# Kernel tuning notes

Hardware: AMD Instinct MI355X
Metric: run time of the kernel (lower is better)

The kernel has to match this reference:

```python
import jax, jax.numpy as jnp
import numpy as np

B, L, D, K, V = 256, 50, 128, 4, 50000
LENGTH = 5      # opt.length
BETA = 0.01     # opt.beta scaling on loss1
EPS = 1e-12     # F.normalize eps


def _l2norm(x, axis):
    n = jnp.sqrt(jnp.sum(x * x, axis=axis, keepdims=True))
    return x / jnp.maximum(n, EPS)


def setup_inputs() -> dict:
    key = jax.random.key(0)
    ks = jax.random.split(key, 11)
    s = 1.0 / np.sqrt(D)  # reset_parameters: uniform(-stdv, stdv)
    u = lambda k, shape: jax.random.uniform(k, shape, jnp.float32, -s, s)
    return {
        "hidden": jax.random.normal(ks[0], (B, L, D), jnp.float32),
        "mask": jnp.ones((B, L), jnp.int32),
        "pos_emb": u(ks[1], (L, D)),
        "w1": u(ks[2], (2 * D, D)),
        "w2": u(ks[3], (D, K)),
        "glu1_w": u(ks[4], (D, K * D)),
        "glu1_b": u(ks[5], (K * D,)),
        "att_w1": u(ks[6], (D, D)),
        "att_w2": u(ks[7], (D, D)),
        "att_v": u(ks[8], (D, K)),
        "emb": u(ks[9], (V, D)),
    }


def reference(hidden, mask, pos_emb, w1, w2, glu1_w, glu1_b, att_w1, att_w2, att_v, emb):
    m = mask.astype(jnp.float32)[..., None]                       # [B,L,1]
    hs = jnp.sum(hidden * m, axis=1) / jnp.sum(m, axis=1)         # [B,D] masked mean
    # nh = tanh(cat(pos, hidden) @ w1); then sigmoid(glu1)
    cat = jnp.concatenate([jnp.broadcast_to(pos_emb[None], hidden.shape), hidden], axis=-1)
    nh = jnp.tanh(cat @ w1)                                       # [B,L,D]
    nh = jax.nn.sigmoid(nh @ glu1_w + glu1_b)                     # [B,L,K*D]
    # torch.split(dim=2) + stack(dim=3) -> [B,L,D,K]
    nh = nh.reshape(B, L, K, D).transpose(0, 1, 3, 2)             # [B,L,D,K]
    beta = jnp.einsum('bldk,dk->blk', nh, w2)                     # [B,L,K]
    # attention gate alpha = sigmoid(att_v(tanh(W1 hs + W2 hidden)))
    att = jnp.tanh(hs[:, None, :] @ att_w1 + hidden @ att_w2)     # [B,L,D]
    alpha = jax.nn.sigmoid(att @ att_v)                           # [B,L,K]
    beta = beta * (0.5 + alpha) * m                               # mask over interests
    # per-interest L2 normalize along sequence (fused over K)
    nb = _l2norm(beta, axis=1)                                    # [B,L,K]
    # pairwise |cos| between interests: vectorized Gram instead of python loops
    G = jnp.einsum('bli,blj->bij', nb, nb)                        # [B,K,K]
    triu = jnp.triu(jnp.ones((K, K), jnp.float32), 1)
    sim = jnp.sum(jnp.abs(G) * triu, axis=(1, 2)) * (2.0 / (K * (K - 1)))  # [B]
    lens = jnp.sum(mask, axis=1).astype(jnp.float32) - LENGTH     # sumask[:,0] - length
    loss1 = jnp.sum(jax.nn.sigmoid(sim * lens))                   # scalar
    # per-interest pooled session reps, stacked on leading axis -> [K,B,D]
    select = jnp.einsum('blk,bld->kbd', beta, hidden)
    b_norm = _l2norm(emb[1:], axis=-1)                            # [V-1,D]
    scores = jnp.einsum('kbd,vd->kbv', select, b_norm)            # [K,B,V-1]
    max_scores = jnp.max(scores, axis=0)                          # [B,V-1]
    return (max_scores, loss1 * BETA, scores)
```

## Files before the change

### kernel.cpp

```cpp
#include <hip/hip_runtime.h>
#include <hip/hip_bf16.h>
#include <math.h>

constexpr int NB = 256;
constexpr int NL = 50;
constexpr int ND = 128;
constexpr int NK = 4;
constexpr int NVm1 = 49999;
constexpr int NPAD2 = 50176;
constexpr int ROWS = NB * NL;
constexpr int MROWS = NB * NK;
constexpr int GEMM_NSPAN = 512;
constexpr int MR = 64;

constexpr int G_BN  = NPAD2 / 8;
constexpr int G_HS  = NB / 2;
constexpr int G_PP  = NL / 2;
constexpr int G_XB  = ROWS * ND / 2048;
constexpr int G_W1T = ND * ND / 256;
constexpr int G_AWT = ND * ND / 256;
constexpr int G_GLT = ND * 512 / 256;
constexpr int G_TOT = G_BN + G_HS + G_PP + G_XB + G_W1T + G_AWT + G_GLT;

typedef __bf16 bf16x8 __attribute__((ext_vector_type(8)));
typedef float f32x4 __attribute__((ext_vector_type(4)));

__device__ __forceinline__ float sigm_fast(float x) { return 1.0f / (1.0f + __expf(-x)); }
__device__ __forceinline__ float sigm_prec(float x) { return 1.0f / (1.0f + expf(-x)); }
__device__ __forceinline__ float fast_tanh(float x) {
    float xc = fminf(fmaxf(x, -15.f), 15.f);
    float e = __expf(2.f * xc);
    return (e - 1.f) / (e + 1.f);
}

__device__ __forceinline__ void gld_lds16(const void* g, void* l) {
    __builtin_amdgcn_global_load_lds(
        (const __attribute__((address_space(1))) void*)g,
        (__attribute__((address_space(3))) void*)l, 16, 0, 0);
}

__global__ __launch_bounds__(256) void k_prep(
    const float* __restrict__ hidden, const int* __restrict__ mask,
    const float* __restrict__ pos_emb, const float* __restrict__ w1,
    const float* __restrict__ att_w2, const float* __restrict__ glu1_w,
    const float* __restrict__ emb,
    float* __restrict__ hs, float* __restrict__ posPart,
    __hip_bfloat16* __restrict__ XbG, __hip_bfloat16* __restrict__ w1h_t,
    __hip_bfloat16* __restrict__ attw2_t, __hip_bfloat16* __restrict__ glu_t,
    __hip_bfloat16* __restrict__ bnv, float* __restrict__ loss_out) {
    __shared__ float sPP[2 * ND];
    int blk = blockIdx.x, tid = threadIdx.x;
    if (blk < G_BN) {
        int v = blk * 8 + (tid >> 5);
        int j = (tid & 31) << 2;
        float4 x = make_float4(0.f, 0.f, 0.f, 0.f);
        if (v < NVm1) x = *(const float4*)&emb[((size_t)v + 1) * ND + j];
        float ss = x.x * x.x + x.y * x.y + x.z * x.z + x.w * x.w;
#pragma unroll
        for (int off = 16; off >= 1; off >>= 1) ss += __shfl_xor(ss, off);
        float rn = 1.f / fmaxf(sqrtf(ss), 1e-12f);
        union { ushort4 u4; __hip_bfloat16 h[4]; } o;
        o.h[0] = __float2bfloat16(x.x * rn);
        o.h[1] = __float2bfloat16(x.y * rn);
        o.h[2] = __float2bfloat16(x.z * rn);
        o.h[3] = __float2bfloat16(x.w * rn);
        *(ushort4*)&bnv[(size_t)v * ND + j] = o.u4;
    } else if (blk < G_BN + G_HS) {
        int b = (blk - G_BN) * 2 + (tid >> 7);
        int d = tid & 127;
        float acc = 0.f, msum = 0.f;
        for (int l = 0; l < NL; ++l) {
            float mv = (float)mask[b * NL + l];
            acc += hidden[((size_t)b * NL + l) * ND + d] * mv;
            msum += mv;
        }
        hs[b * ND + d] = acc / msum;
        if (blk == G_BN && tid == 0) loss_out[0] = 0.f;
    } else if (blk < G_BN + G_HS + G_PP) {
        int rel = blk - (G_BN + G_HS);
        int rl = tid >> 7, d = tid & 127;
        int r = rel * 2 + rl;
        sPP[rl * ND + d] = pos_emb[r * ND + d];
        __syncthreads();
        float acc = 0.f;
#pragma unroll 8
        for (int j = 0; j < ND; ++j) acc += sPP[rl * ND + j] * w1[j * ND + d];
        posPart[r * ND + d] = acc;
    } else if (blk < G_BN + G_HS + G_PP + G_XB) {
        int rel = blk - (G_BN + G_HS + G_PP);
        size_t base = (size_t)rel * 2048 + (size_t)tid * 8;
        float4 f0 = *(const float4*)&hidden[base];
        float4 f1 = *(const float4*)&hidden[base + 4];
        union { bf16x8 v; __hip_bfloat16 h[8]; } u;
        u.h[0] = __float2bfloat16(f0.x); u.h[1] = __float2bfloat16(f0.y);
        u.h[2] = __float2bfloat16(f0.z); u.h[3] = __float2bfloat16(f0.w);
        u.h[4] = __float2bfloat16(f1.x); u.h[5] = __float2bfloat16(f1.y);
        u.h[6] = __float2bfloat16(f1.z); u.h[7] = __float2bfloat16(f1.w);
        *(bf16x8*)&XbG[base] = u.v;
    } else if (blk < G_BN + G_HS + G_PP + G_XB + G_W1T) {
        int i = (blk - (G_BN + G_HS + G_PP + G_XB)) * 256 + tid;
        int d = i >> 7, j = i & 127;
        w1h_t[d * ND + j] = __float2bfloat16(w1[(ND + j) * ND + d]);
    } else if (blk < G_BN + G_HS + G_PP + G_XB + G_W1T + G_AWT) {
        int i = (blk - (G_BN + G_HS + G_PP + G_XB + G_W1T)) * 256 + tid;
        int d = i >> 7, j = i & 127;
        attw2_t[d * ND + j] = __float2bfloat16(att_w2[j * ND + d]);
    } else {
        int i = (blk - (G_BN + G_HS + G_PP + G_XB + G_W1T + G_AWT)) * 256 + tid;
        int c = i >> 7, j = i & 127;
        glu_t[c * ND + j] = __float2bfloat16(glu1_w[j * 512 + c]);
    }
}

__global__ __launch_bounds__(256) void k_mega(
    const __hip_bfloat16* __restrict__ XbG, const __hip_bfloat16* __restrict__ w1h_t,
    const __hip_bfloat16* __restrict__ attw2_t, const __hip_bfloat16* __restrict__ glu_t,
    const float* __restrict__ hs, const float* __restrict__ att_w1,
    const float* __restrict__ att_v, const float* __restrict__ posPart,
    const float* __restrict__ glu1_b, const float* __restrict__ w2,
    const int* __restrict__ mask, float* __restrict__ beta_out) {
    __shared__ __hip_bfloat16 XbS[MR * ND];
    __shared__ __hip_bfloat16 WS[ND * ND];
    __shared__ __attribute__((aligned(16))) __hip_bfloat16 NHS[MR * 136];
    __shared__ float alphaS[MR * NK];
    __shared__ float hsW1S[3 * ND];
    int row0 = blockIdx.x * MR;
    int tid = threadIdx.x;
    int wave = tid >> 6, lane = tid & 63, l16 = lane & 15, quad = lane >> 4;
    int b0 = row0 / NL;

#pragma unroll
    for (int it = 0; it < 4; ++it) {
        int id = it * 256 + tid;
        int row = id >> 4, c = id & 15, gc = c ^ (row & 7);
        gld_lds16((const char*)XbG + ((size_t)(row0 + row) * 16 + gc) * 16,
                  (char*)XbS + (size_t)(it * 256 + wave * 64) * 16);
    }
#pragma unroll
    for (int it = 0; it < 8; ++it) {
        int id = it * 256 + tid;
        int row = id >> 4, c = id & 15, gc = c ^ (row & 7);
        gld_lds16((const char*)attw2_t + ((size_t)row * 16 + gc) * 16,
                  (char*)WS + (size_t)(it * 256 + wave * 64) * 16);
    }
    for (int i = tid; i < 3 * ND; i += 256) {
        int bb = i >> 7, d = i & 127, b = b0 + bb;
        float acc = 0.f;
        if (b < NB) {
            for (int j = 0; j < ND; ++j) acc += hs[b * ND + j] * att_w1[j * ND + d];
        }
        hsW1S[i] = acc;
    }
    __syncthreads();

    const bf16x8* Xv = (const bf16x8*)XbS;
    const bf16x8* Wv = (const bf16x8*)WS;
    const bf16x8* Nv = (const bf16x8*)NHS;
    int arow = wave * 16 + l16;

    f32x4 acc8[8];
#pragma unroll
    for (int ni = 0; ni < 8; ++ni) acc8[ni] = (f32x4){0.f, 0.f, 0.f, 0.f};
#pragma unroll
    for (int kk = 0; kk < 4; ++kk) {
        int ko = kk * 4 + quad;
        bf16x8 af = Xv[arow * 16 + (ko ^ (arow & 7))];
#pragma unroll
        for (int ni = 0; ni < 8; ++ni) {
            int n = ni * 16 + l16;
            bf16x8 bf = Wv[n * 16 + (ko ^ (n & 7))];
            acc8[ni] = __builtin_amdgcn_mfma_f32_16x16x32_bf16(af, bf, acc8[ni], 0, 0, 0);
        }
    }
#pragma unroll
    for (int r = 0; r < 4; ++r) {
        int lrow = wave * 16 + quad * 4 + r;
        int grow = row0 + lrow;
        int bb = grow / NL - b0;
        float a0 = 0.f, a1 = 0.f, a2 = 0.f, a3 = 0.f;
#pragma unroll
        for (int ni = 0; ni < 8; ++ni) {
            int col = ni * 16 + l16;
            float atv = fast_tanh(hsW1S[bb * ND + col] + acc8[ni][r]);
            float4 av = *(const float4*)&att_v[col * 4];
            a0 += atv * av.x; a1 += atv * av.y; a2 += atv * av.z; a3 += atv * av.w;
        }
#pragma unroll
        for (int off = 1; off < 16; off <<= 1) {
            a0 += __shfl_xor(a0, off); a1 += __shfl_xor(a1, off);
            a2 += __shfl_xor(a2, off); a3 += __shfl_xor(a3, off);
        }
        if (l16 == 0) {
            alphaS[lrow * 4 + 0] = sigm_fast(a0);
            alphaS[lrow * 4 + 1] = sigm_fast(a1);
            alphaS[lrow * 4 + 2] = sigm_fast(a2);
            alphaS[lrow * 4 + 3] = sigm_fast(a3);
        }
    }
    __syncthreads();
#pragma unroll
    for (int it = 0; it < 8; ++it) {
        int id = it * 256 + tid;
        int row = id >> 4, c = id & 15, gc = c ^ (row & 7);
        gld_lds16((const char*)w1h_t + ((size_t)row * 16 + gc) * 16,
                  (char*)WS + (size_t)(it * 256 + wave * 64) * 16);
    }
    __syncthreads();
#pragma unroll
    for (int ni = 0; ni < 8; ++ni) acc8[ni] = (f32x4){0.f, 0.f, 0.f, 0.f};
#pragma unroll
    for (int kk = 0; kk < 4; ++kk) {
        int ko = kk * 4 + quad;
        bf16x8 af = Xv[arow * 16 + (ko ^ (arow & 7))];
#pragma unroll
        for (int ni = 0; ni < 8; ++ni) {
            int n = ni * 16 + l16;
            bf16x8 bf = Wv[n * 16 + (ko ^ (n & 7))];
            acc8[ni] = __builtin_amdgcn_mfma_f32_16x16x32_bf16(af, bf, acc8[ni], 0, 0, 0);
        }
    }
#pragma unroll
    for (int r = 0; r < 4; ++r) {
        int lrow = wave * 16 + quad * 4 + r;
        int grow = row0 + lrow;
        int l = grow % NL;
#pragma unroll
        for (int ni = 0; ni < 8; ++ni) {
            int col = ni * 16 + l16;
            float nhv = fast_tanh(posPart[l * ND + col] + acc8[ni][r]);
            NHS[lrow * 136 + col] = __float2bfloat16(nhv);
        }
    }
    __syncthreads();
    for (int ch = 0; ch < 4; ++ch) {
#pragma unroll
        for (int it = 0; it < 8; ++it) {
            int id = it * 256 + tid;
            int row = id >> 4, c = id & 15, gc = c ^ (row & 7);
            gld_lds16((const char*)glu_t + ((size_t)(ch * ND + row) * 16 + gc) * 16,
                      (char*)WS + (size_t)(it * 256 + wave * 64) * 16);
        }
        __syncthreads();
#pragma unroll
        for (int ni = 0; ni < 8; ++ni) acc8[ni] = (f32x4){0.f, 0.f, 0.f, 0.f};
#pragma unroll
        for (int kk = 0; kk < 4; ++kk) {
            int ko = kk * 4 + quad;
            bf16x8 af = Nv[arow * 17 + ko];
#pragma unroll
            for (int ni = 0; ni < 8; ++ni) {
                int n = ni * 16 + l16;
                bf16x8 bf = Wv[n * 16 + (ko ^ (n & 7))];
                acc8[ni] = __builtin_amdgcn_mfma_f32_16x16x32_bf16(af, bf, acc8[ni], 0, 0, 0);
            }
        }
#pragma unroll
        for (int r = 0; r < 4; ++r) {
            float s = 0.f;
#pragma unroll
            for (int ni = 0; ni < 8; ++ni) {
                int col = ni * 16 + l16;
                s += sigm_fast(acc8[ni][r] + glu1_b[ch * ND + col]) * w2[col * 4 + ch];
            }
#pragma unroll
            for (int off = 1; off < 16; off <<= 1) s += __shfl_xor(s, off);
            if (l16 == 0) {
                int lrow = wave * 16 + quad * 4 + r;
                int grow = row0 + lrow;
                float a = alphaS[lrow * 4 + ch];
                beta_out[(size_t)grow * 4 + ch] = s * (0.5f + a) * (float)mask[grow];
            }
        }
        __syncthreads();
    }
}

__global__ void k_loss(const float* __restrict__ beta, const int* __restrict__ mask,
                       float* __restrict__ loss_out) {
    int b = blockIdx.x;
    int t = threadIdx.x;
    float mv = (t < NL) ? (float)mask[b * NL + t] : 0.f;
    float msum = mv;
    for (int off = 32; off >= 1; off >>= 1) msum += __shfl_xor(msum, off);
    float lens = msum - 5.0f;
    float bk[NK] = {0.f, 0.f, 0.f, 0.f};
    if (t < NL) {
#pragma unroll
        for (int k = 0; k < NK; ++k) bk[k] = beta[((size_t)b * NL + t) * NK + k];
    }
    float nb[NK];
#pragma unroll
    for (int k = 0; k < NK; ++k) {
        float v = bk[k] * bk[k];
        for (int off = 32; off >= 1; off >>= 1) v += __shfl_xor(v, off);
        nb[k] = bk[k] / fmaxf(sqrtf(v), 1e-12f);
    }
    float sim = 0.f;
#pragma unroll
    for (int i = 0; i < NK; ++i) {
#pragma unroll
        for (int j = 0; j < NK; ++j) {
            if (j > i) {
                float p = nb[i] * nb[j];
                for (int off = 32; off >= 1; off >>= 1) p += __shfl_xor(p, off);
                sim += fabsf(p);
            }
        }
    }
    sim *= (2.0f / (NK * (NK - 1)));
    if (t == 0) atomicAdd(loss_out, sigm_prec(sim * lens) * 0.01f);
}

__global__ __launch_bounds__(256) void k_select(
    const float* __restrict__ beta, const float* __restrict__ hidden,
    __hip_bfloat16* __restrict__ selb) {
    int b = blockIdx.x * 2 + (threadIdx.x >> 7);
    int d = threadIdx.x & 127;
    float a0 = 0.f, a1 = 0.f, a2 = 0.f, a3 = 0.f;
    for (int l = 0; l < NL; ++l) {
        float h = hidden[((size_t)b * NL + l) * ND + d];
        float4 bv = *(const float4*)&beta[((size_t)b * NL + l) * NK];
        a0 = fmaf(bv.x, h, a0);
        a1 = fmaf(bv.y, h, a1);
        a2 = fmaf(bv.z, h, a2);
        a3 = fmaf(bv.w, h, a3);
    }
    selb[((size_t)b * NK + 0) * ND + d] = __float2bfloat16(a0);
    selb[((size_t)b * NK + 1) * ND + d] = __float2bfloat16(a1);
    selb[((size_t)b * NK + 2) * ND + d] = __float2bfloat16(a2);
    selb[((size_t)b * NK + 3) * ND + d] = __float2bfloat16(a3);
}

__global__ __launch_bounds__(256) void k_gemm(
    const __hip_bfloat16* __restrict__ selb, const __hip_bfloat16* __restrict__ bn,
    float* __restrict__ scores, float* __restrict__ maxs) {
    __shared__ __attribute__((aligned(16))) __hip_bfloat16 As[128 * 128];
    __shared__ __attribute__((aligned(16))) __hip_bfloat16 Bs[2][64 * 128];
    int bm0 = blockIdx.y * 128;
    int nbase = blockIdx.x * GEMM_NSPAN;
    int tid = threadIdx.x;
    int wave = tid >> 6, lane = tid & 63;
    int l16 = lane & 15, quad = lane >> 4;
    int m_loc = wave * 32;
    bool full = (nbase + GEMM_NSPAN) <= NVm1;
    const size_t SC_K = (size_t)NB * NVm1;

#pragma unroll
    for (int it = 0; it < 8; ++it) {
        int id = it * 256 + tid;
        int row = id >> 4, c = id & 15, gc = c ^ (row & 7);
        gld_lds16((const char*)selb + ((size_t)(bm0 + row) * 16 + gc) * 16,
                  (char*)As + (size_t)(it * 256 + wave * 64) * 16);
    }
#pragma unroll
    for (int it = 0; it < 4; ++it) {
        int id = it * 256 + tid;
        int row = id >> 4, c = id & 15, gc = c ^ (row & 7);
        gld_lds16((const char*)bn + ((size_t)(nbase + row) * 16 + gc) * 16,
                  (char*)Bs[0] + (size_t)(it * 256 + wave * 64) * 16);
    }
    __syncthreads();

    const bf16x8* Av = (const bf16x8*)As;

#pragma unroll
    for (int ch = 0; ch < 8; ++ch) {
        if (ch < 7) {
            int bn0 = nbase + (ch + 1) * 64;
#pragma unroll
            for (int it = 0; it < 4; ++it) {
                int id = it * 256 + tid;
                int row = id >> 4, c = id & 15, gc = c ^ (row & 7);
                gld_lds16((const char*)bn + ((size_t)(bn0 + row) * 16 + gc) * 16,
                          (char*)Bs[(ch + 1) & 1] + (size_t)(it * 256 + wave * 64) * 16);
            }
            __builtin_amdgcn_sched_barrier(0);
        }
        const bf16x8* Bv = (const bf16x8*)Bs[ch & 1];
        f32x4 acc[2][4];
#pragma unroll
        for (int mi = 0; mi < 2; ++mi)
#pragma unroll
            for (int ni = 0; ni < 4; ++ni) acc[mi][ni] = (f32x4){0.f, 0.f, 0.f, 0.f};

#pragma unroll
        for (int kk = 0; kk < 4; ++kk) {
            int ko = kk * 4 + quad;
            bf16x8 afr[2], bfr[4];
#pragma unroll
            for (int mi = 0; mi < 2; ++mi) {
                int row = m_loc + mi * 16 + l16;
                afr[mi] = Av[row * 16 + (ko ^ (row & 7))];
            }
#pragma unroll
            for (int ni = 0; ni < 4; ++ni) {
                int row = ni * 16 + l16;
                bfr[ni] = Bv[row * 16 + (ko ^ (row & 7))];
            }
#pragma unroll
            for (int mi = 0; mi < 2; ++mi)
#pragma unroll
                for (int ni = 0; ni < 4; ++ni)
                    acc[mi][ni] = __builtin_amdgcn_mfma_f32_16x16x32_bf16(
                        afr[mi], bfr[ni], acc[mi][ni], 0, 0, 0);
        }

        int ncol0 = nbase + ch * 64;
#pragma unroll
        for (int mi = 0; mi < 2; ++mi) {
            int m_base = bm0 + m_loc + mi * 16;
            int bidx = (m_base >> 2) + quad;
#pragma unroll
            for (int ni = 0; ni < 4; ++ni) {
                int n = ncol0 + ni * 16 + l16;
                if (full || n < NVm1) {
                    float mx = acc[mi][ni][0];
#pragma unroll
                    for (int r = 0; r < 4; ++r) {
                        float val = acc[mi][ni][r];
                        scores[(size_t)r * SC_K + (size_t)bidx * NVm1 + n] = val;
                        mx = fmaxf(mx, val);
                    }
                    maxs[(size_t)bidx * NVm1 + n] = mx;
                }
            }
        }

        if (ch < 7) {
            if (full) {
                asm volatile("s_waitcnt vmcnt(40) lgkmcnt(0)" ::: "memory");
                __builtin_amdgcn_s_barrier();
            } else {
                __syncthreads();
            }
        }
    }
}

extern "C" void kernel_launch(void* const* d_in, const int* in_sizes, int n_in,
                              void* d_out, int out_size, void* d_ws, size_t ws_size,
                              hipStream_t stream) {
    const float* hidden  = (const float*)d_in[0];
    const int*   mask    = (const int*)d_in[1];
    const float* pos_emb = (const float*)d_in[2];
    const float* w1      = (const float*)d_in[3];
    const float* w2      = (const float*)d_in[4];
    const float* glu1_w  = (const float*)d_in[5];
    const float* glu1_b  = (const float*)d_in[6];
    const float* att_w1  = (const float*)d_in[7];
    const float* att_w2  = (const float*)d_in[8];
    const float* att_v   = (const float*)d_in[9];
    const float* emb     = (const float*)d_in[10];

    float* out      = (float*)d_out;
    float* max_out  = out;
    float* loss_out = out + (size_t)NB * NVm1;
    float* scores   = out + (size_t)NB * NVm1 + 1;

    char* w = (char*)d_ws;
    auto alloc = [&](size_t bytes) {
        char* p = w;
        w += (bytes + 255) & ~(size_t)255;
        return p;
    };
    float* posPart = (float*)alloc((size_t)NL * ND * 4);
    float* hs      = (float*)alloc((size_t)NB * ND * 4);
    float* betav   = (float*)alloc((size_t)ROWS * NK * 4);
    __hip_bfloat16* XbG     = (__hip_bfloat16*)alloc((size_t)ROWS * ND * 2);
    __hip_bfloat16* w1h_t   = (__hip_bfloat16*)alloc((size_t)ND * ND * 2);
    __hip_bfloat16* attw2_t = (__hip_bfloat16*)alloc((size_t)ND * ND * 2);
    __hip_bfloat16* glu_t   = (__hip_bfloat16*)alloc((size_t)512 * ND * 2);
    __hip_bfloat16* selb    = (__hip_bfloat16*)alloc((size_t)MROWS * ND * 2);
    __hip_bfloat16* bnv     = (__hip_bfloat16*)alloc((size_t)NPAD2 * ND * 2);

    k_prep<<<G_TOT, 256, 0, stream>>>(hidden, mask, pos_emb, w1, att_w2, glu1_w, emb,
                                      hs, posPart, XbG, w1h_t, attw2_t, glu_t, bnv, loss_out);
    k_mega<<<ROWS / MR, 256, 0, stream>>>(XbG, w1h_t, attw2_t, glu_t, hs, att_w1,
                                          att_v, posPart, glu1_b, w2, mask, betav);
    k_loss<<<NB, 64, 0, stream>>>(betav, mask, loss_out);
    k_select<<<NB / 2, 256, 0, stream>>>(betav, hidden, selb);
    k_gemm<<<dim3(NPAD2 / GEMM_NSPAN, MROWS / 128), 256, 0, stream>>>(selb, bnv, scores, max_out);
}
```

Baseline: 432.4 us.

## Precompute hs@att_w1 in prep; restructure score GEMM with swapped operands and vector stores

```diff
diff --git a/kernel.cpp b/kernel.cpp
--- a/kernel.cpp
+++ b/kernel.cpp
@@ -14,16 +14,17 @@
 constexpr int MR = 64;
 
 constexpr int G_BN  = NPAD2 / 8;
-constexpr int G_HS  = NB / 2;
+constexpr int G_HW  = NB / 2;
 constexpr int G_PP  = NL / 2;
 constexpr int G_XB  = ROWS * ND / 2048;
 constexpr int G_W1T = ND * ND / 256;
 constexpr int G_AWT = ND * ND / 256;
 constexpr int G_GLT = ND * 512 / 256;
-constexpr int G_TOT = G_BN + G_HS + G_PP + G_XB + G_W1T + G_AWT + G_GLT;
+constexpr int G_TOT = G_BN + G_HW + G_PP + G_XB + G_W1T + G_AWT + G_GLT;
 
 typedef __bf16 bf16x8 __attribute__((ext_vector_type(8)));
 typedef float f32x4 __attribute__((ext_vector_type(4)));
+typedef f32x4 f32x4u __attribute__((aligned(4)));
 
 __device__ __forceinline__ float sigm_fast(float x) { return 1.0f / (1.0f + __expf(-x)); }
 __device__ __forceinline__ float sigm_prec(float x) { return 1.0f / (1.0f + expf(-x)); }
@@ -42,9 +43,9 @@
 __global__ __launch_bounds__(256) void k_prep(
     const float* __restrict__ hidden, const int* __restrict__ mask,
     const float* __restrict__ pos_emb, const float* __restrict__ w1,
-    const float* __restrict__ att_w2, const float* __restrict__ glu1_w,
-    const float* __restrict__ emb,
-    float* __restrict__ hs, float* __restrict__ posPart,
+    const float* __restrict__ att_w1, const float* __restrict__ att_w2,
+    const float* __restrict__ glu1_w, const float* __restrict__ emb,
+    float* __restrict__ hsW1, float* __restrict__ posPart,
     __hip_bfloat16* __restrict__ XbG, __hip_bfloat16* __restrict__ w1h_t,
     __hip_bfloat16* __restrict__ attw2_t, __hip_bfloat16* __restrict__ glu_t,
     __hip_bfloat16* __restrict__ bnv, float* __restrict__ loss_out) {
@@ -65,19 +66,24 @@
         o.h[2] = __float2bfloat16(x.z * rn);
         o.h[3] = __float2bfloat16(x.w * rn);
         *(ushort4*)&bnv[(size_t)v * ND + j] = o.u4;
-    } else if (blk < G_BN + G_HS) {
-        int b = (blk - G_BN) * 2 + (tid >> 7);
-        int d = tid & 127;
+    } else if (blk < G_BN + G_HW) {
+        int half = tid >> 7, d = tid & 127;
+        int b = (blk - G_BN) * 2 + half;
         float acc = 0.f, msum = 0.f;
         for (int l = 0; l < NL; ++l) {
             float mv = (float)mask[b * NL + l];
             acc += hidden[((size_t)b * NL + l) * ND + d] * mv;
             msum += mv;
         }
-        hs[b * ND + d] = acc / msum;
+        sPP[half * ND + d] = acc / msum;
+        __syncthreads();
+        float o = 0.f;
+#pragma unroll 8
+        for (int j = 0; j < ND; ++j) o += sPP[half * ND + j] * att_w1[j * ND + d];
+        hsW1[b * ND + d] = o;
         if (blk == G_BN && tid == 0) loss_out[0] = 0.f;
-    } else if (blk < G_BN + G_HS + G_PP) {
-        int rel = blk - (G_BN + G_HS);
+    } else if (blk < G_BN + G_HW + G_PP) {
+        int rel = blk - (G_BN + G_HW);
         int rl = tid >> 7, d = tid & 127;
         int r = rel * 2 + rl;
         sPP[rl * ND + d] = pos_emb[r * ND + d];
@@ -86,8 +92,8 @@
 #pragma unroll 8
         for (int j = 0; j < ND; ++j) acc += sPP[rl * ND + j] * w1[j * ND + d];
         posPart[r * ND + d] = acc;
-    } else if (blk < G_BN + G_HS + G_PP + G_XB) {
-        int rel = blk - (G_BN + G_HS + G_PP);
+    } else if (blk < G_BN + G_HW + G_PP + G_XB) {
+        int rel = blk - (G_BN + G_HW + G_PP);
         size_t base = (size_t)rel * 2048 + (size_t)tid * 8;
         float4 f0 = *(const float4*)&hidden[base];
         float4 f1 = *(const float4*)&hidden[base + 4];
@@ -97,16 +103,16 @@
         u.h[4] = __float2bfloat16(f1.x); u.h[5] = __float2bfloat16(f1.y);
         u.h[6] = __float2bfloat16(f1.z); u.h[7] = __float2bfloat16(f1.w);
         *(bf16x8*)&XbG[base] = u.v;
-    } else if (blk < G_BN + G_HS + G_PP + G_XB + G_W1T) {
-        int i = (blk - (G_BN + G_HS + G_PP + G_XB)) * 256 + tid;
+    } else if (blk < G_BN + G_HW + G_PP + G_XB + G_W1T) {
+        int i = (blk - (G_BN + G_HW + G_PP + G_XB)) * 256 + tid;
         int d = i >> 7, j = i & 127;
         w1h_t[d * ND + j] = __float2bfloat16(w1[(ND + j) * ND + d]);
-    } else if (blk < G_BN + G_HS + G_PP + G_XB + G_W1T + G_AWT) {
-        int i = (blk - (G_BN + G_HS + G_PP + G_XB + G_W1T)) * 256 + tid;
+    } else if (blk < G_BN + G_HW + G_PP + G_XB + G_W1T + G_AWT) {
+        int i = (blk - (G_BN + G_HW + G_PP + G_XB + G_W1T)) * 256 + tid;
         int d = i >> 7, j = i & 127;
         attw2_t[d * ND + j] = __float2bfloat16(att_w2[j * ND + d]);
     } else {
-        int i = (blk - (G_BN + G_HS + G_PP + G_XB + G_W1T + G_AWT)) * 256 + tid;
+        int i = (blk - (G_BN + G_HW + G_PP + G_XB + G_W1T + G_AWT)) * 256 + tid;
         int c = i >> 7, j = i & 127;
         glu_t[c * ND + j] = __float2bfloat16(glu1_w[j * 512 + c]);
     }
@@ -115,10 +121,10 @@
 __global__ __launch_bounds__(256) void k_mega(
     const __hip_bfloat16* __restrict__ XbG, const __hip_bfloat16* __restrict__ w1h_t,
     const __hip_bfloat16* __restrict__ attw2_t, const __hip_bfloat16* __restrict__ glu_t,
-    const float* __restrict__ hs, const float* __restrict__ att_w1,
-    const float* __restrict__ att_v, const float* __restrict__ posPart,
-    const float* __restrict__ glu1_b, const float* __restrict__ w2,
-    const int* __restrict__ mask, float* __restrict__ beta_out) {
+    const float* __restrict__ hsW1, const float* __restrict__ att_v,
+    const float* __restrict__ posPart, const float* __restrict__ glu1_b,
+    const float* __restrict__ w2, const int* __restrict__ mask,
+    float* __restrict__ beta_out) {
     __shared__ __hip_bfloat16 XbS[MR * ND];
     __shared__ __hip_bfloat16 WS[ND * ND];
     __shared__ __attribute__((aligned(16))) __hip_bfloat16 NHS[MR * 136];
@@ -144,12 +150,8 @@
                   (char*)WS + (size_t)(it * 256 + wave * 64) * 16);
     }
     for (int i = tid; i < 3 * ND; i += 256) {
-        int bb = i >> 7, d = i & 127, b = b0 + bb;
-        float acc = 0.f;
-        if (b < NB) {
-            for (int j = 0; j < ND; ++j) acc += hs[b * ND + j] * att_w1[j * ND + d];
-        }
-        hsW1S[i] = acc;
+        int b = b0 + (i >> 7);
+        hsW1S[i] = (b < NB) ? hsW1[b * ND + (i & 127)] : 0.f;
     }
     __syncthreads();
 
@@ -334,19 +336,19 @@
 __global__ __launch_bounds__(256) void k_gemm(
     const __hip_bfloat16* __restrict__ selb, const __hip_bfloat16* __restrict__ bn,
     float* __restrict__ scores, float* __restrict__ maxs) {
-    __shared__ __attribute__((aligned(16))) __hip_bfloat16 As[128 * 128];
+    __shared__ __attribute__((aligned(16))) __hip_bfloat16 As[64 * 128];
     __shared__ __attribute__((aligned(16))) __hip_bfloat16 Bs[2][64 * 128];
-    int bm0 = blockIdx.y * 128;
+    int bm0 = blockIdx.y * 64;
     int nbase = blockIdx.x * GEMM_NSPAN;
     int tid = threadIdx.x;
     int wave = tid >> 6, lane = tid & 63;
     int l16 = lane & 15, quad = lane >> 4;
-    int m_loc = wave * 32;
+    int m_loc = wave * 16;
     bool full = (nbase + GEMM_NSPAN) <= NVm1;
     const size_t SC_K = (size_t)NB * NVm1;
 
 #pragma unroll
-    for (int it = 0; it < 8; ++it) {
+    for (int it = 0; it < 4; ++it) {
         int id = it * 256 + tid;
         int row = id >> 4, c = id & 15, gc = c ^ (row & 7);
         gld_lds16((const char*)selb + ((size_t)(bm0 + row) * 16 + gc) * 16,
@@ -362,6 +364,16 @@
     __syncthreads();
 
     const bf16x8* Av = (const bf16x8*)As;
+    bf16x8 sf[4];
+#pragma unroll
+    for (int kk = 0; kk < 4; ++kk) {
+        int row = m_loc + l16, ko = kk * 4 + quad;
+        sf[kk] = Av[row * 16 + (ko ^ (row & 7))];
+    }
+
+    f32x4 acc[32];
+#pragma unroll
+    for (int i = 0; i < 32; ++i) acc[i] = (f32x4){0.f, 0.f, 0.f, 0.f};
 
 #pragma unroll
     for (int ch = 0; ch < 8; ++ch) {
@@ -374,64 +386,59 @@
                 gld_lds16((const char*)bn + ((size_t)(bn0 + row) * 16 + gc) * 16,
                           (char*)Bs[(ch + 1) & 1] + (size_t)(it * 256 + wave * 64) * 16);
             }
-            __builtin_amdgcn_sched_barrier(0);
         }
         const bf16x8* Bv = (const bf16x8*)Bs[ch & 1];
-        f32x4 acc[2][4];
-#pragma unroll
-        for (int mi = 0; mi < 2; ++mi)
-#pragma unroll
-            for (int ni = 0; ni < 4; ++ni) acc[mi][ni] = (f32x4){0.f, 0.f, 0.f, 0.f};
-
 #pragma unroll
         for (int kk = 0; kk < 4; ++kk) {
             int ko = kk * 4 + quad;
-            bf16x8 afr[2], bfr[4];
-#pragma unroll
-            for (int mi = 0; mi < 2; ++mi) {
-                int row = m_loc + mi * 16 + l16;
-                afr[mi] = Av[row * 16 + (ko ^ (row & 7))];
-            }
+            bf16x8 af[4];
 #pragma unroll
             for (int ni = 0; ni < 4; ++ni) {
                 int row = ni * 16 + l16;
-                bfr[ni] = Bv[row * 16 + (ko ^ (row & 7))];
-            }
-#pragma unroll
-            for (int mi = 0; mi < 2; ++mi)
-#pragma unroll
-                for (int ni = 0; ni < 4; ++ni)
-                    acc[mi][ni] = __builtin_amdgcn_mfma_f32_16x16x32_bf16(
-                        afr[mi], bfr[ni], acc[mi][ni], 0, 0, 0);
-        }
-
-        int ncol0 = nbase + ch * 64;
-#pragma unroll
-        for (int mi = 0; mi < 2; ++mi) {
-            int m_base = bm0 + m_loc + mi * 16;
-            int bidx = (m_base >> 2) + quad;
-#pragma unroll
-            for (int ni = 0; ni < 4; ++ni) {
-                int n = ncol0 + ni * 16 + l16;
-                if (full || n < NVm1) {
-                    float mx = acc[mi][ni][0];
-#pragma unroll
-                    for (int r = 0; r < 4; ++r) {
-                        float val = acc[mi][ni][r];
-                        scores[(size_t)r * SC_K + (size_t)bidx * NVm1 + n] = val;
-                        mx = fmaxf(mx, val);
-                    }
-                    maxs[(size_t)bidx * NVm1 + n] = mx;
+                af[ni] = Bv[row * 16 + (ko ^ (row & 7))];
+            }
+#pragma unroll
+            for (int ni = 0; ni < 4; ++ni)
+                acc[ch * 4 + ni] = __builtin_amdgcn_mfma_f32_16x16x32_bf16(
+                    af[ni], sf[kk], acc[ch * 4 + ni], 0, 0, 0);
+        }
+        __syncthreads();
+    }
+
+    int m = bm0 + m_loc + l16;
+    float* srow = scores + (size_t)(l16 & 3) * SC_K + (size_t)(m >> 2) * NVm1;
+    float* mrow = maxs + (size_t)(m >> 2) * NVm1;
+    if (full) {
+#pragma unroll
+        for (int ni = 0; ni < 32; ++ni) {
+            int n0 = nbase + ni * 16 + quad * 4;
+            f32x4 v = acc[ni];
+            *(f32x4u*)&srow[n0] = v;
+            f32x4 w;
+#pragma unroll
+            for (int c = 0; c < 4; ++c) {
+                float t = fmaxf(v[c], __shfl_xor(v[c], 1));
+                w[c] = fmaxf(t, __shfl_xor(t, 2));
+            }
+            if ((l16 & 3) == 0) *(f32x4u*)&mrow[n0] = w;
+        }
+    } else {
+#pragma unroll
+        for (int ni = 0; ni < 32; ++ni) {
+            int n0 = nbase + ni * 16 + quad * 4;
+            f32x4 v = acc[ni];
+            f32x4 w;
+#pragma unroll
+            for (int c = 0; c < 4; ++c) {
+                float t = fmaxf(v[c], __shfl_xor(v[c], 1));
+                w[c] = fmaxf(t, __shfl_xor(t, 2));
+            }
+#pragma unroll
+            for (int c = 0; c < 4; ++c) {
+                if (n0 + c < NVm1) {
+                    srow[n0 + c] = v[c];
+                    if ((l16 & 3) == 0) mrow[n0 + c] = w[c];
                 }
-            }
-        }
-
-        if (ch < 7) {
-            if (full) {
-                asm volatile("s_waitcnt vmcnt(40) lgkmcnt(0)" ::: "memory");
-                __builtin_amdgcn_s_barrier();
-            } else {
-                __syncthreads();
             }
         }
     }
@@ -464,7 +471,7 @@
         return p;
     };
     float* posPart = (float*)alloc((size_t)NL * ND * 4);
-    float* hs      = (float*)alloc((size_t)NB * ND * 4);
+    float* hsW1    = (float*)alloc((size_t)NB * ND * 4);
     float* betav   = (float*)alloc((size_t)ROWS * NK * 4);
     __hip_bfloat16* XbG     = (__hip_bfloat16*)alloc((size_t)ROWS * ND * 2);
     __hip_bfloat16* w1h_t   = (__hip_bfloat16*)alloc((size_t)ND * ND * 2);
@@ -473,11 +480,12 @@
     __hip_bfloat16* selb    = (__hip_bfloat16*)alloc((size_t)MROWS * ND * 2);
     __hip_bfloat16* bnv     = (__hip_bfloat16*)alloc((size_t)NPAD2 * ND * 2);
 
-    k_prep<<<G_TOT, 256, 0, stream>>>(hidden, mask, pos_emb, w1, att_w2, glu1_w, emb,
-                                      hs, posPart, XbG, w1h_t, attw2_t, glu_t, bnv, loss_out);
-    k_mega<<<ROWS / MR, 256, 0, stream>>>(XbG, w1h_t, attw2_t, glu_t, hs, att_w1,
+    k_prep<<<G_TOT, 256, 0, stream>>>(hidden, mask, pos_emb, w1, att_w1, att_w2, glu1_w,
+                                      emb, hsW1, posPart, XbG, w1h_t, attw2_t, glu_t,
+                                      bnv, loss_out);
+    k_mega<<<ROWS / MR, 256, 0, stream>>>(XbG, w1h_t, attw2_t, glu_t, hsW1,
                                           att_v, posPart, glu1_b, w2, mask, betav);
     k_loss<<<NB, 64, 0, stream>>>(betav, mask, loss_out);
     k_select<<<NB / 2, 256, 0, stream>>>(betav, hidden, selb);
-    k_gemm<<<dim3(NPAD2 / GEMM_NSPAN, MROWS / 128), 256, 0, stream>>>(selb, bnv, scores, max_out);
-}
+    k_gemm<<<dim3(NPAD2 / GEMM_NSPAN, MROWS / 64), 256, 0, stream>>>(selb, bnv, scores, max_out);
+}
```

After: 420.8 us. 1.03x faster.
